# Kernel optimization log

Measured on AMD Instinct MI355X. Metric: run time of the kernel, lower is better.

The kernel has to match this reference:

```python
import jax, jax.numpy as jnp
import numpy as np

N_NODES = 100000


def graph_conv(x, edge_index, w_rel, b_rel, w_root):
    # PyG GraphConv (aggr='add'): out = lin_rel(sum_{j in N(i)} x_j) + lin_root(x_i)
    src = edge_index[0]
    dst = edge_index[1]
    msgs = x[src]                                   # [E, F] gather
    agg = jax.ops.segment_sum(msgs, dst, num_segments=N_NODES)  # [N, F] scatter-add
    return agg @ w_rel.T + b_rel + x @ w_root.T


def setup_inputs() -> dict:
    key = jax.random.key(0)
    k_x, k_e, k1, k2, k3, k4, k5 = jax.random.split(key, 7)
    input_dim, hidden_dim, output_dim = 128, 128, 64
    n_edges = 1600000
    x = jax.random.normal(k_x, (N_NODES, input_dim), dtype=jnp.float32)
    edge_index = jax.random.randint(k_e, (2, n_edges), 0, N_NODES, dtype=jnp.int64)
    s1 = 1.0 / np.sqrt(input_dim)
    s2 = 1.0 / np.sqrt(hidden_dim)
    return {
        "x": x,
        "edge_index": edge_index,
        "w_rel1": jax.random.uniform(k1, (hidden_dim, input_dim), jnp.float32, -s1, s1),
        "b_rel1": jax.random.uniform(k2, (hidden_dim,), jnp.float32, -s1, s1),
        "w_root1": jax.random.uniform(k3, (hidden_dim, input_dim), jnp.float32, -s1, s1),
        "w_rel2": jax.random.uniform(k4, (output_dim, hidden_dim), jnp.float32, -s2, s2),
        "b_rel2": jax.random.uniform(k5, (output_dim,), jnp.float32, -s2, s2),
        "w_root2": jax.random.uniform(jax.random.fold_in(key, 9), (output_dim, hidden_dim), jnp.float32, -s2, s2),
    }


def reference(x, edge_index, w_rel1, b_rel1, w_root1, w_rel2, b_rel2, w_root2):
    h = graph_conv(x, edge_index, w_rel1, b_rel1, w_root1)  # conv1
    h = jax.nn.relu(h)
    out = graph_conv(h, edge_index, w_rel2, b_rel2, w_root2)  # conv2
    return out
```

## Files before the change

### kernel.cpp

```cpp
#include <hip/hip_runtime.h>


typedef float f4 __attribute__((ext_vector_type(4)));
typedef _Float16 h8 __attribute__((ext_vector_type(8)));
typedef _Float16 h2 __attribute__((ext_vector_type(2)));

#define NB   1024
#define EPB  4096

__device__ __forceinline__ float2 h2f(unsigned u) {
    h2 p = __builtin_bit_cast(h2, u);
    float2 r; r.x = (float)p[0]; r.y = (float)p[1];
    return r;
}
__device__ __forceinline__ unsigned f2h(float a, float b) {
    h2 p; p[0] = (_Float16)a; p[1] = (_Float16)b;
    return __builtin_bit_cast(unsigned, p);
}

__global__ void wcast(const float* __restrict__ wr1, const float* __restrict__ wq1,
                      const float* __restrict__ wr2, const float* __restrict__ wq2,
                      _Float16* __restrict__ wb)
{
    int i = blockIdx.x * 256 + threadIdx.x;
    if (i < 16384)      wb[i] = (_Float16)wr1[i];
    else if (i < 32768) wb[i] = (_Float16)wq1[i - 16384];
    else if (i < 40960) wb[i] = (_Float16)wr2[i - 32768];
    else if (i < 49152) wb[i] = (_Float16)wq2[i - 40960];
}

__global__ void xcast(const float* __restrict__ x, _Float16* __restrict__ xh,
                      long n)
{
    long i = (long)(blockIdx.x * 256 + threadIdx.x) * 8;
    if (i >= n) return;
    f4 a = *(const f4*)(x + i);
    f4 b = *(const f4*)(x + i + 4);
    h8 o;
    o[0] = (_Float16)a[0]; o[1] = (_Float16)a[1];
    o[2] = (_Float16)a[2]; o[3] = (_Float16)a[3];
    o[4] = (_Float16)b[0]; o[5] = (_Float16)b[1];
    o[6] = (_Float16)b[2]; o[7] = (_Float16)b[3];
    *(h8*)(xh + i) = o;
}

__global__ __launch_bounds__(256) void s1_hist(const int* __restrict__ dst,
                                               int* __restrict__ mat, int E)
{
    __shared__ int hist[NB];
    const int tid = threadIdx.x;
    for (int i = tid; i < NB; i += 256) hist[i] = 0;
    __syncthreads();
    const int e0 = blockIdx.x * EPB;
#pragma unroll
    for (int it = 0; it < EPB / 256; ++it) {
        int e = e0 + it * 256 + tid;
        if (e < E) atomicAdd(&hist[dst[e] >> 7], 1);
    }
    __syncthreads();
    int* row = mat + (size_t)blockIdx.x * NB;
    for (int i = tid; i < NB; i += 256) row[i] = hist[i];
}

__global__ __launch_bounds__(512) void s2_colscan(int* __restrict__ mat,
                                                  int* __restrict__ tot, int nblk)
{
    __shared__ int ts[512];
    const int tid = threadIdx.x;
    const int b = blockIdx.x;
    int v = (tid < nblk) ? mat[(size_t)tid * NB + b] : 0;
    ts[tid] = v;
    __syncthreads();
#pragma unroll
    for (int off = 1; off < 512; off <<= 1) {
        int add = (tid >= off) ? ts[tid - off] : 0;
        __syncthreads();
        ts[tid] += add;
        __syncthreads();
    }
    if (tid < nblk) mat[(size_t)tid * NB + b] = ts[tid] - v;
    if (tid == 511) tot[b] = ts[511];
}

__global__ __launch_bounds__(NB) void s2b_base(const int* __restrict__ tot,
                                               int* __restrict__ bb,
                                               int* __restrict__ row_ptr,
                                               int N, int E)
{
    __shared__ int ts[NB];
    const int tid = threadIdx.x;
    int v = tot[tid];
    ts[tid] = v;
    __syncthreads();
#pragma unroll
    for (int off = 1; off < NB; off <<= 1) {
        int add = (tid >= off) ? ts[tid - off] : 0;
        __syncthreads();
        ts[tid] += add;
        __syncthreads();
    }
    bb[tid] = ts[tid] - v;
    if (tid == NB - 1) { bb[NB] = ts[NB - 1]; row_ptr[N] = E; }
}

__global__ __launch_bounds__(256) void s3_scatter(const int* __restrict__ src,
                                                  const int* __restrict__ dst,
                                                  const int* __restrict__ mat,
                                                  const int* __restrict__ bb,
                                                  unsigned* __restrict__ coarse, int E)
{
    __shared__ int cur[NB];
    const int tid = threadIdx.x;
    const int* mrow = mat + (size_t)blockIdx.x * NB;
    for (int i = tid; i < NB; i += 256) cur[i] = bb[i] + mrow[i];
    __syncthreads();
    const int e0 = blockIdx.x * EPB;
#pragma unroll
    for (int it = 0; it < EPB / 256; ++it) {
        int e = e0 + it * 256 + tid;
        if (e < E) {
            int d = dst[e];
            int p = atomicAdd(&cur[d >> 7], 1);
            coarse[p] = ((unsigned)src[e] << 7) | (unsigned)(d & 127);
        }
    }
}

__global__ __launch_bounds__(256) void s4_fine(const unsigned* __restrict__ coarse,
                                               const int* __restrict__ bb,
                                               int* __restrict__ row_ptr,
                                               int* __restrict__ srcs, int N)
{
    __shared__ int fcnt[128];
    __shared__ int fs[128];
    __shared__ int cur[128];
    const int tid = threadIdx.x;
    const int b = blockIdx.x;
    const int seg0 = bb[b], seg1 = bb[b + 1];
    if (tid < 128) fcnt[tid] = 0;
    __syncthreads();
    for (int p = seg0 + tid; p < seg1; p += 256)
        atomicAdd(&fcnt[coarse[p] & 127u], 1);
    __syncthreads();
    if (tid < 128) fs[tid] = fcnt[tid];
    __syncthreads();
#pragma unroll
    for (int off = 1; off < 128; off <<= 1) {
        int add = 0;
        if (tid < 128 && tid >= off) add = fs[tid - off];
        __syncthreads();
        if (tid < 128) fs[tid] += add;
        __syncthreads();
    }
    if (tid < 128) {
        int excl = fs[tid] - fcnt[tid];
        cur[tid] = seg0 + excl;
        int d = b * 128 + tid;
        if (d < N) row_ptr[d] = seg0 + excl;
    }
    __syncthreads();
    for (int p = seg0 + tid; p < seg1; p += 256) {
        unsigned v = coarse[p];
        int q = atomicAdd(&cur[v & 127u], 1);
        srcs[q] = (int)(v >> 7);
    }
}

__global__ __launch_bounds__(256) void pull_h128(const uint2* __restrict__ xh4,
                                                 const int* __restrict__ row_ptr,
                                                 const int* __restrict__ srcs,
                                                 uint2* __restrict__ aggh4, int N)
{
    const int w    = (blockIdx.x * 256 + threadIdx.x) >> 6;
    const int l    = threadIdx.x & 63;
    const int half = l >> 5;
    const int col  = l & 31;
    if (w >= N) return;
    const int beg = row_ptr[w], end = row_ptr[w + 1];
    float a0 = 0.f, a1 = 0.f, a2 = 0.f, a3 = 0.f;
    int j = beg;
    for (; j + 7 < end; j += 8) {
        int s0 = srcs[j + 0 + half], s1 = srcs[j + 2 + half];
        int s2 = srcs[j + 4 + half], s3 = srcs[j + 6 + half];
        uint2 u0 = xh4[(size_t)s0 * 32 + col];
        uint2 u1 = xh4[(size_t)s1 * 32 + col];
        uint2 u2 = xh4[(size_t)s2 * 32 + col];
        uint2 u3 = xh4[(size_t)s3 * 32 + col];
        float2 p;
        p = h2f(u0.x); a0 += p.x; a1 += p.y;  p = h2f(u0.y); a2 += p.x; a3 += p.y;
        p = h2f(u1.x); a0 += p.x; a1 += p.y;  p = h2f(u1.y); a2 += p.x; a3 += p.y;
        p = h2f(u2.x); a0 += p.x; a1 += p.y;  p = h2f(u2.y); a2 += p.x; a3 += p.y;
        p = h2f(u3.x); a0 += p.x; a1 += p.y;  p = h2f(u3.y); a2 += p.x; a3 += p.y;
    }
    for (; j < end; j += 2) {
        int jj = j + half;
        float m = (jj < end) ? 1.f : 0.f;
        int s = srcs[(jj < end) ? jj : (end - 1)];
        uint2 u = xh4[(size_t)s * 32 + col];
        float2 p;
        p = h2f(u.x); a0 += m * p.x; a1 += m * p.y;
        p = h2f(u.y); a2 += m * p.x; a3 += m * p.y;
    }
    a0 += __shfl_xor(a0, 32); a1 += __shfl_xor(a1, 32);
    a2 += __shfl_xor(a2, 32); a3 += __shfl_xor(a3, 32);
    if (half == 0) {
        uint2 o; o.x = f2h(a0, a1); o.y = f2h(a2, a3);
        aggh4[(size_t)w * 32 + col] = o;
    }
}

__global__ __launch_bounds__(256) void pull_add_h64(const uint2* __restrict__ hr4,
                                                    const int* __restrict__ row_ptr,
                                                    const int* __restrict__ srcs,
                                                    float* __restrict__ out, int N)
{
    const int w   = (blockIdx.x * 256 + threadIdx.x) >> 6;
    const int l   = threadIdx.x & 63;
    const int q   = l >> 4;
    const int col = l & 15;
    if (w >= N) return;
    const int beg = row_ptr[w], end = row_ptr[w + 1];
    float a0 = 0.f, a1 = 0.f, a2 = 0.f, a3 = 0.f;
    int j = beg;
    for (; j + 7 < end; j += 8) {
        int s0 = srcs[j + q], s1 = srcs[j + 4 + q];
        uint2 u0 = hr4[(size_t)s0 * 16 + col];
        uint2 u1 = hr4[(size_t)s1 * 16 + col];
        float2 p;
        p = h2f(u0.x); a0 += p.x; a1 += p.y;  p = h2f(u0.y); a2 += p.x; a3 += p.y;
        p = h2f(u1.x); a0 += p.x; a1 += p.y;  p = h2f(u1.y); a2 += p.x; a3 += p.y;
    }
    for (; j < end; j += 4) {
        int jj = j + q;
        float m = (jj < end) ? 1.f : 0.f;
        int s = srcs[(jj < end) ? jj : (end - 1)];
        uint2 u = hr4[(size_t)s * 16 + col];
        float2 p;
        p = h2f(u.x); a0 += m * p.x; a1 += m * p.y;
        p = h2f(u.y); a2 += m * p.x; a3 += m * p.y;
    }
    a0 += __shfl_xor(a0, 16); a1 += __shfl_xor(a1, 16);
    a2 += __shfl_xor(a2, 16); a3 += __shfl_xor(a3, 16);
    a0 += __shfl_xor(a0, 32); a1 += __shfl_xor(a1, 32);
    a2 += __shfl_xor(a2, 32); a3 += __shfl_xor(a3, 32);
    if (q == 0) {
        f4* po = (f4*)out + (size_t)w * 16 + col;
        f4 cur = *po;
        cur[0] += a0; cur[1] += a1; cur[2] += a2; cur[3] += a3;
        *po = cur;
    }
}

__global__ __launch_bounds__(512) void mfma_fused(
    const _Float16* __restrict__ aggh, const _Float16* __restrict__ xh,
    const _Float16* __restrict__ wb,
    const float* __restrict__ b1, const float* __restrict__ b2,
    _Float16* __restrict__ hrh, float* __restrict__ outp, int N)
{
    __shared__ _Float16 smem[49152 + 8 * 16 * 128];
    _Float16* lw = smem;
    const int tid = threadIdx.x;
    const int wv = tid >> 6;
    const int l  = tid & 63;
    const int lr = l & 15;
    const int kg = l >> 4;
    _Float16* hb = smem + 49152 + wv * (16 * 128);

#pragma unroll
    for (int it = 0; it < 12; ++it) {
        int g = tid + it * 512;
        int d = (g & ~15) | ((g ^ (g >> 4)) & 15);
        *(h8*)&lw[d * 8] = *(const h8*)(wb + (size_t)g * 8);
    }
    __syncthreads();

    const int ntiles = (N + 127) / 128;
    for (int t = blockIdx.x; t < ntiles; t += gridDim.x) {
        const int base = t * 128 + wv * 16;
        const int r0 = min(base + lr, N - 1);

        h8 afr[8];
#pragma unroll
        for (int c = 0; c < 4; ++c) {
            const int k0 = c * 32 + kg * 8;
            afr[c]     = *(const h8*)(aggh + (size_t)r0 * 128 + k0);
            afr[c + 4] = *(const h8*)(xh   + (size_t)r0 * 128 + k0);
        }

        f4 acc[8];
#pragma unroll
        for (int n = 0; n < 8; ++n) acc[n] = 0.f;
#pragma unroll
        for (int kk = 0; kk < 8; ++kk) {
            const int R = (kk < 4) ? 0 : 16384;
            const int sl = ((kk & 3) * 4 + kg) ^ lr;
#pragma unroll
            for (int n = 0; n < 8; ++n) {
                h8 bf = *(const h8*)&lw[R + (n * 16 + lr) * 128 + (sl << 3)];
                acc[n] = __builtin_amdgcn_mfma_f32_16x16x32_f16(afr[kk], bf, acc[n], 0, 0, 0);
            }
        }

        const int ro = kg * 4;
#pragma unroll
        for (int n = 0; n < 8; ++n) {
            const int col = n * 16 + lr;
            const float bias = b1[col];
#pragma unroll
            for (int j = 0; j < 4; ++j) {
                const int row = ro + j;
                hb[row * 128 + (col ^ ((row & 7) << 3))] =
                    (_Float16)fmaxf(acc[n][j] + bias, 0.f);
            }
        }

        f4 acc2[8];
#pragma unroll
        for (int n = 0; n < 8; ++n) acc2[n] = 0.f;
#pragma unroll
        for (int kk = 0; kk < 4; ++kk) {
            const int k0 = kk * 32 + kg * 8;
            const int swz = (lr & 7) << 3;
            h8 a0 = *(const h8*)&hb[lr * 128 + (k0 ^ swz)];
            const int sl = (kk * 4 + kg) ^ lr;
#pragma unroll
            for (int n = 0; n < 8; ++n) {
                const int R2 = (n < 4) ? 32768 : 40960;
                h8 bf = *(const h8*)&lw[R2 + ((n & 3) * 16 + lr) * 128 + (sl << 3)];
                acc2[n] = __builtin_amdgcn_mfma_f32_16x16x32_f16(a0, bf, acc2[n], 0, 0, 0);
            }
        }

#pragma unroll
        for (int n = 0; n < 8; ++n) {
            const int col = n * 16 + lr;
#pragma unroll
            for (int j = 0; j < 4; ++j) {
                int r = base + ro + j;
                if (r < N) {
                    if (n < 4) {
                        hrh[(size_t)r * 64 + col] = (_Float16)acc2[n][j];
                    } else {
                        outp[(size_t)r * 64 + (col - 64)] = acc2[n][j] + b2[col - 64];
                    }
                }
            }
        }
    }
}

extern "C" void kernel_launch(void* const* d_in, const int* in_sizes, int n_in,
                              void* d_out, int out_size, void* d_ws, size_t ws_size,
                              hipStream_t stream)
{
    const float* x       = (const float*)d_in[0];
    const int*   ei      = (const int*)d_in[1];
    const float* w_rel1  = (const float*)d_in[2];
    const float* b_rel1  = (const float*)d_in[3];
    const float* w_root1 = (const float*)d_in[4];
    const float* w_rel2  = (const float*)d_in[5];
    const float* b_rel2  = (const float*)d_in[6];
    const float* w_root2 = (const float*)d_in[7];
    float* out = (float*)d_out;

    const int N = in_sizes[0] / 128;
    const int E = in_sizes[1] / 2;
    const int* src = ei;
    const int* dst = ei + E;

    _Float16* xh    = (_Float16*)d_ws;
    _Float16* aggh  = xh + (size_t)N * 128;
    _Float16* hrh   = aggh;
    _Float16* wbuf  = aggh + (size_t)N * 128;
    int*      srcs    = (int*)(wbuf + 49152);
    unsigned* coarse  = (unsigned*)(srcs + E);
    const int nblk    = (E + EPB - 1) / EPB;
    int*      mat     = (int*)(coarse + E);
    int*      tot     = mat + (size_t)nblk * NB;
    int*      bb      = tot + NB;
    int*      row_ptr = bb + (NB + 1);

    wcast<<<(49152 + 255) / 256, 256, 0, stream>>>(w_rel1, w_root1, w_rel2, w_root2, wbuf);
    xcast<<<(N * 128 / 8 + 255) / 256, 256, 0, stream>>>(x, xh, (long)N * 128);

    s1_hist   <<<nblk, 256, 0, stream>>>(dst, mat, E);
    s2_colscan<<<NB, 512, 0, stream>>>(mat, tot, nblk);
    s2b_base  <<<1, NB, 0, stream>>>(tot, bb, row_ptr, N, E);
    s3_scatter<<<nblk, 256, 0, stream>>>(src, dst, mat, bb, coarse, E);
    s4_fine   <<<NB, 256, 0, stream>>>(coarse, bb, row_ptr, srcs, N);

    pull_h128<<<(N * 64 + 255) / 256, 256, 0, stream>>>(
        (const uint2*)xh, row_ptr, srcs, (uint2*)aggh, N);

    mfma_fused<<<256, 512, 0, stream>>>(
        aggh, xh, wbuf, b_rel1, b_rel2, hrh, out, N);

    pull_add_h64<<<(N * 64 + 255) / 256, 256, 0, stream>>>(
        (const uint2*)hrh, row_ptr, srcs, out, N);
}
```

Measured before the change: 206.5 us.

## Fuse weight/x casts into histogram kernel and prefetch next tile in MFMA loop

The separate weight-cast and x-cast kernels are merged into the histogram kernel, which now also converts x to fp16 with a grid-stride loop and casts the weights in its first 24 blocks. This removes two kernel launches and lets the cast traffic overlap the histogram atomics. The fused MFMA kernel also loads the next tile's A fragments into registers before computing the current tile, to hide global load latency. The prefetch raises register pressure and issues one redundant clamped load on the last iteration.

After: 205.9 us. No clear change (-0.3%).

```diff
diff --git a/kernel.cpp b/kernel.cpp
--- a/kernel.cpp
+++ b/kernel.cpp
@@ -18,34 +18,12 @@
     return __builtin_bit_cast(unsigned, p);
 }
 
-__global__ void wcast(const float* __restrict__ wr1, const float* __restrict__ wq1,
-                      const float* __restrict__ wr2, const float* __restrict__ wq2,
-                      _Float16* __restrict__ wb)
-{
-    int i = blockIdx.x * 256 + threadIdx.x;
-    if (i < 16384)      wb[i] = (_Float16)wr1[i];
-    else if (i < 32768) wb[i] = (_Float16)wq1[i - 16384];
-    else if (i < 40960) wb[i] = (_Float16)wr2[i - 32768];
-    else if (i < 49152) wb[i] = (_Float16)wq2[i - 40960];
-}
-
-__global__ void xcast(const float* __restrict__ x, _Float16* __restrict__ xh,
-                      long n)
-{
-    long i = (long)(blockIdx.x * 256 + threadIdx.x) * 8;
-    if (i >= n) return;
-    f4 a = *(const f4*)(x + i);
-    f4 b = *(const f4*)(x + i + 4);
-    h8 o;
-    o[0] = (_Float16)a[0]; o[1] = (_Float16)a[1];
-    o[2] = (_Float16)a[2]; o[3] = (_Float16)a[3];
-    o[4] = (_Float16)b[0]; o[5] = (_Float16)b[1];
-    o[6] = (_Float16)b[2]; o[7] = (_Float16)b[3];
-    *(h8*)(xh + i) = o;
-}
-
-__global__ __launch_bounds__(256) void s1_hist(const int* __restrict__ dst,
-                                               int* __restrict__ mat, int E)
+__global__ __launch_bounds__(256) void prep_fused(
+    const int* __restrict__ dst, int* __restrict__ mat,
+    const float* __restrict__ x, _Float16* __restrict__ xh,
+    const float* __restrict__ wr1, const float* __restrict__ wq1,
+    const float* __restrict__ wr2, const float* __restrict__ wq2,
+    _Float16* __restrict__ wb, int E, long nxchunks)
 {
     __shared__ int hist[NB];
     const int tid = threadIdx.x;
@@ -56,6 +34,31 @@
     for (int it = 0; it < EPB / 256; ++it) {
         int e = e0 + it * 256 + tid;
         if (e < E) atomicAdd(&hist[dst[e] >> 7], 1);
+    }
+    const long stride = (long)gridDim.x * 256;
+    for (long c = (long)blockIdx.x * 256 + tid; c < nxchunks; c += stride) {
+        const float* p = x + c * 8;
+        f4 a = *(const f4*)p;
+        f4 b = *(const f4*)(p + 4);
+        h8 o;
+        o[0] = (_Float16)a[0]; o[1] = (_Float16)a[1];
+        o[2] = (_Float16)a[2]; o[3] = (_Float16)a[3];
+        o[4] = (_Float16)b[0]; o[5] = (_Float16)b[1];
+        o[6] = (_Float16)b[2]; o[7] = (_Float16)b[3];
+        *(h8*)(xh + c * 8) = o;
+    }
+    if (blockIdx.x < 24) {
+        int i = (blockIdx.x * 256 + tid) * 8;
+#pragma unroll
+        for (int k = 0; k < 8; ++k) {
+            int j = i + k;
+            _Float16 v;
+            if (j < 16384)      v = (_Float16)wr1[j];
+            else if (j < 32768) v = (_Float16)wq1[j - 16384];
+            else if (j < 40960) v = (_Float16)wr2[j - 32768];
+            else                v = (_Float16)wq2[j - 40960];
+            wb[j] = v;
+        }
     }
     __syncthreads();
     int* row = mat + (size_t)blockIdx.x * NB;
@@ -275,17 +278,35 @@
     __syncthreads();
 
     const int ntiles = (N + 127) / 128;
-    for (int t = blockIdx.x; t < ntiles; t += gridDim.x) {
-        const int base = t * 128 + wv * 16;
-        const int r0 = min(base + lr, N - 1);
-
-        h8 afr[8];
+    const int ro = kg * 4;
+
+    int t = blockIdx.x;
+    h8 afr[8];
+    {
+        const int r0 = min(t * 128 + wv * 16 + lr, N - 1);
 #pragma unroll
         for (int c = 0; c < 4; ++c) {
             const int k0 = c * 32 + kg * 8;
             afr[c]     = *(const h8*)(aggh + (size_t)r0 * 128 + k0);
             afr[c + 4] = *(const h8*)(xh   + (size_t)r0 * 128 + k0);
         }
+    }
+
+    for (; t < ntiles; ) {
+        const int base = t * 128 + wv * 16;
+        const int tn = t + gridDim.x;
+        const int tc = min(tn, ntiles - 1);
+
+        h8 nxt[8];
+        {
+            const int rn = min(tc * 128 + wv * 16 + lr, N - 1);
+#pragma unroll
+            for (int c = 0; c < 4; ++c) {
+                const int k0 = c * 32 + kg * 8;
+                nxt[c]     = *(const h8*)(aggh + (size_t)rn * 128 + k0);
+                nxt[c + 4] = *(const h8*)(xh   + (size_t)rn * 128 + k0);
+            }
+        }
 
         f4 acc[8];
 #pragma unroll
@@ -301,7 +322,6 @@
             }
         }
 
-        const int ro = kg * 4;
 #pragma unroll
         for (int n = 0; n < 8; ++n) {
             const int col = n * 16 + lr;
@@ -346,6 +366,10 @@
                 }
             }
         }
+
+#pragma unroll
+        for (int c = 0; c < 8; ++c) afr[c] = nxt[c];
+        t = tn;
     }
 }
 
@@ -380,10 +404,10 @@
     int*      bb      = tot + NB;
     int*      row_ptr = bb + (NB + 1);
 
-    wcast<<<(49152 + 255) / 256, 256, 0, stream>>>(w_rel1, w_root1, w_rel2, w_root2, wbuf);
-    xcast<<<(N * 128 / 8 + 255) / 256, 256, 0, stream>>>(x, xh, (long)N * 128);
-
-    s1_hist   <<<nblk, 256, 0, stream>>>(dst, mat, E);
+    prep_fused<<<nblk, 256, 0, stream>>>(dst, mat, x, xh,
+                                         w_rel1, w_root1, w_rel2, w_root2,
+                                         wbuf, E, (long)N * 16);
+
     s2_colscan<<<NB, 512, 0, stream>>>(mat, tot, nblk);
     s2b_base  <<<1, NB, 0, stream>>>(tot, bb, row_ptr, N, E);
     s3_scatter<<<nblk, 256, 0, stream>>>(src, dst, mat, bb, coarse, E);
```
